# Kernel optimization log

Measured on AMD Instinct MI355X. Metric: run time of the kernel, lower is better.

The kernel has to match this reference:

```python
import jax, jax.numpy as jnp
import numpy as np
from jax import lax

NUM_KP = 17
MAX_PEOPLE = 30
HEAT_THRESH = 0.1
STRIDE = 4  # heatmap -> image coordinate scale

def setup_inputs() -> dict:
    key = jax.random.key(0)
    heatmaps = jax.random.uniform(key, (32, NUM_KP, 256, 256), dtype=jnp.float32)
    return {"heatmaps": heatmaps}

def reference(heatmaps):
    # heatmaps: [B, C, H, W]
    B, C, H, W = heatmaps.shape
    neg_inf = jnp.float32(-jnp.inf)
    # 3x3 max-pool NMS (stride 1, pad 1) batched over all B*C channels at once.
    hmax = lax.reduce_window(
        heatmaps, neg_inf, lax.max,
        window_dimensions=(1, 1, 3, 3),
        window_strides=(1, 1, 1, 1),
        padding=((0, 0), (0, 0), (1, 1), (1, 1)),
    )
    nms = heatmaps * (hmax == heatmaps).astype(heatmaps.dtype)
    # Threshold + descending sort + take top max_people, done as a batched top_k.
    flat = nms.reshape(B, C, H * W)
    masked = jnp.where(flat > HEAT_THRESH, flat, neg_inf)
    scores, idx = lax.top_k(masked, MAX_PEOPLE)          # [B, C, max_people]
    y = idx // W
    x = idx % W
    coords = jnp.stack([x, y], axis=-1).astype(jnp.int32) * STRIDE  # [B,C,max_people,2] as (x,y)*4
    valid = scores > HEAT_THRESH                          # padding mask (original output is ragged)
    return coords, scores, valid
```

## Files before the change

kernel.cpp:

```cpp
#include <hip/hip_runtime.h>
#include <stdint.h>

#define NUM_KP 17
#define BATCH  32
#define HDIM   256
#define WDIM   256
#define NCH    (BATCH * NUM_KP)
#define MAXP   30
#define CAP    8192

#define NBINS  4096
#define QB     125953

__device__ __forceinline__ unsigned long long shfl_down_u64(unsigned long long v, int off) {
    unsigned lo = (unsigned)v, hi = (unsigned)(v >> 32);
    lo = __shfl_down(lo, off);
    hi = __shfl_down(hi, off);
    return ((unsigned long long)hi << 32) | lo;
}
__device__ __forceinline__ unsigned long long shfl_u64(unsigned long long v, int lane) {
    unsigned lo = (unsigned)v, hi = (unsigned)(v >> 32);
    lo = __shfl(lo, lane);
    hi = __shfl(hi, lane);
    return ((unsigned long long)hi << 32) | lo;
}
__device__ __forceinline__ unsigned quant12(float v) {
    int b = (int)(__float_as_uint(v) >> 13) - QB;
    b = b < 1 ? 1 : (b > NBINS - 1 ? NBINS - 1 : b);
    return (unsigned)b;
}

__global__ __launch_bounds__(256)
void pose_fused_kernel(const float* __restrict__ heat, float* __restrict__ out, int out_size) {
    __shared__ unsigned s_buf[CAP];
    __shared__ int s_hist[NBINS];
    __shared__ int s_gsum[256];
    __shared__ unsigned long long s_ref[256];
    __shared__ int s_cnt, s_nref, s_tau;

    const int tid  = threadIdx.x;
    const int chan = blockIdx.x;
    const int wave = tid >> 6;
    const int lane = tid & 63;
    const float NEGINF = -__builtin_inff();
    const float* __restrict__ cp = heat + (size_t)chan * (HDIM * WDIM);

    for (int i = tid; i < NBINS; i += 256) s_hist[i] = 0;
    if (tid == 0) { s_cnt = 0; s_nref = 0; }
    __syncthreads();

    const int r0 = wave << 6;
    const float* colp = cp + (lane << 2);
    const float4 NEG4 = make_float4(NEGINF, NEGINF, NEGINF, NEGINF);

    float4 rm = (r0 > 0) ? *(const float4*)(colp + ((r0 - 1) << 8)) : NEG4;
    float4 rc = *(const float4*)(colp + (r0 << 8));

    for (int rr = 0; rr < 64; ++rr) {
        const int r = r0 + rr;
        float4 rp = (r + 1 < HDIM) ? *(const float4*)(colp + ((r + 1) << 8)) : NEG4;

        float vm0 = fmaxf(rm.x, fmaxf(rc.x, rp.x));
        float vm1 = fmaxf(rm.y, fmaxf(rc.y, rp.y));
        float vm2 = fmaxf(rm.z, fmaxf(rc.z, rp.z));
        float vm3 = fmaxf(rm.w, fmaxf(rc.w, rp.w));
        float left  = __shfl_up(vm3, 1);   if (lane == 0)  left  = NEGINF;
        float right = __shfl_down(vm0, 1); if (lane == 63) right = NEGINF;
        float h0 = fmaxf(left, fmaxf(vm0, vm1));
        float h1 = fmaxf(vm0, fmaxf(vm1, vm2));
        float h2 = fmaxf(vm1, fmaxf(vm2, vm3));
        float h3 = fmaxf(vm2, fmaxf(vm3, right));

        const int base = (r << 8) | (lane << 2);
        if (rc.x > 0.1f && rc.x == h0) {
            int pos = atomicAdd(&s_cnt, 1);
            if (pos < CAP) s_buf[pos] = (quant12(rc.x) << 16) | (unsigned)(base + 0);
        }
        if (rc.y > 0.1f && rc.y == h1) {
            int pos = atomicAdd(&s_cnt, 1);
            if (pos < CAP) s_buf[pos] = (quant12(rc.y) << 16) | (unsigned)(base + 1);
        }
        if (rc.z > 0.1f && rc.z == h2) {
            int pos = atomicAdd(&s_cnt, 1);
            if (pos < CAP) s_buf[pos] = (quant12(rc.z) << 16) | (unsigned)(base + 2);
        }
        if (rc.w > 0.1f && rc.w == h3) {
            int pos = atomicAdd(&s_cnt, 1);
            if (pos < CAP) s_buf[pos] = (quant12(rc.w) << 16) | (unsigned)(base + 3);
        }
        rm = rc; rc = rp;
    }
    __syncthreads();

    const int n = s_cnt < CAP ? s_cnt : CAP;
    for (int i = tid; i < n; i += 256) {
        atomicAdd(&s_hist[s_buf[i] >> 16], 1);
    }
    __syncthreads();

    {
        int s = 0;
        #pragma unroll
        for (int j = 0; j < 16; ++j) s += s_hist[tid * 16 + j];
        s_gsum[tid] = s;
    }
    __syncthreads();
    if (tid == 0) {
        int cum = 0, tau = 0;
        for (int g = 255; g >= 0; --g) {
            int gs = s_gsum[g];
            if (cum + gs >= MAXP) {
                for (int b = g * 16 + 15; b >= g * 16; --b) {
                    cum += s_hist[b];
                    if (cum >= MAXP) { tau = b; break; }
                }
                break;
            }
            cum += gs;
        }
        s_tau = tau;
    }
    __syncthreads();

    const unsigned tau = (unsigned)s_tau;
    for (int i = tid; i < n; i += 256) {
        unsigned p = s_buf[i];
        if ((p >> 16) >= tau) {
            int pos = atomicAdd(&s_nref, 1);
            if (pos < 256) {
                unsigned idx = p & 0xFFFFu;
                float sc = cp[idx];
                s_ref[pos] = ((unsigned long long)__float_as_uint(sc) << 32) | (unsigned)(~idx);
            }
        }
    }
    __syncthreads();
    const int nref = s_nref < 256 ? s_nref : 256;

    if (tid < 64) {
        unsigned long long k0 = (tid       < nref) ? s_ref[tid]       : 0ull;
        unsigned long long k1 = (tid + 64  < nref) ? s_ref[tid + 64]  : 0ull;
        unsigned long long k2 = (tid + 128 < nref) ? s_ref[tid + 128] : 0ull;
        unsigned long long k3 = (tid + 192 < nref) ? s_ref[tid + 192] : 0ull;
        for (int r = 0; r < MAXP; ++r) {
            unsigned long long best = k0; int bs = 0;
            if (k1 > best) { best = k1; bs = 1; }
            if (k2 > best) { best = k2; bs = 2; }
            if (k3 > best) { best = k3; bs = 3; }
            unsigned long long key = best;
            int slot = (bs << 6) | tid;
            #pragma unroll
            for (int off = 32; off > 0; off >>= 1) {
                unsigned long long ok = shfl_down_u64(key, off);
                int os = __shfl_down(slot, off);
                if (ok > key) { key = ok; slot = os; }
            }
            key  = shfl_u64(key, 0);
            slot = __shfl(slot, 0);
            if ((slot & 63) == tid) {
                int which = slot >> 6;
                if      (which == 0) k0 = 0ull;
                else if (which == 1) k1 = 0ull;
                else if (which == 2) k2 = 0ull;
                else                 k3 = 0ull;
            }
            if (tid == 0) {
                float sc, vld; unsigned idx;
                if (key != 0ull) {
                    sc  = __uint_as_float((unsigned)(key >> 32));
                    idx = (~(unsigned)key) & 0xFFFFu;
                    vld = 1.0f;
                } else { sc = NEGINF; idx = 0u; vld = 0.0f; }
                int x = (int)(idx & 255), y = (int)(idx >> 8);
                long long cb = ((long long)chan * MAXP + r) * 2;
                if (cb + 1 < out_size) {
                    out[cb]     = (float)(x * 4);
                    out[cb + 1] = (float)(y * 4);
                }
                long long so = (long long)NCH * MAXP * 2 + (long long)chan * MAXP + r;
                if (so < out_size) out[so] = sc;
                long long vo = (long long)NCH * MAXP * 3 + (long long)chan * MAXP + r;
                if (vo < out_size) out[vo] = vld;
            }
        }
    }
}

extern "C" void kernel_launch(void* const* d_in, const int* in_sizes, int n_in,
                              void* d_out, int out_size, void* d_ws, size_t ws_size,
                              hipStream_t stream) {
    const float* heat = (const float*)d_in[0];
    float* out = (float*)d_out;
    hipLaunchKernelGGL(pose_fused_kernel, dim3(NCH), dim3(256), 0, stream, heat, out, out_size);
}
```

Measured before the change: 259.9 us.

## Use 512 threads, wave-aggregated ballot compaction, and batched row loads in NMS scan

Doubles the block to 512 threads so each wave scans 32 rows instead of 64. Per-element shared atomics are replaced by ballot/popcount compaction with a single atomic per wave per row. Rows are loaded four at a time ahead of use to give more memory-level parallelism. The intent is to cut LDS atomic contention and hide global load latency. In exchange the unrolled loop raises register pressure, and the larger block may limit occupancy given the large shared memory footprint.

After: 238.1 us. -8.4%, faster.

```diff
diff --git a/kernel.cpp b/kernel.cpp
--- a/kernel.cpp
+++ b/kernel.cpp
@@ -12,6 +12,8 @@
 #define NBINS  4096
 #define QB     125953
 
+#define THREADS 512
+
 __device__ __forceinline__ unsigned long long shfl_down_u64(unsigned long long v, int off) {
     unsigned lo = (unsigned)v, hi = (unsigned)(v >> 32);
     lo = __shfl_down(lo, off);
@@ -30,7 +32,7 @@
     return (unsigned)b;
 }
 
-__global__ __launch_bounds__(256)
+__global__ __launch_bounds__(THREADS, 4)
 void pose_fused_kernel(const float* __restrict__ heat, float* __restrict__ out, int out_size) {
     __shared__ unsigned s_buf[CAP];
     __shared__ int s_hist[NBINS];
@@ -45,25 +47,24 @@
     const float NEGINF = -__builtin_inff();
     const float* __restrict__ cp = heat + (size_t)chan * (HDIM * WDIM);
 
-    for (int i = tid; i < NBINS; i += 256) s_hist[i] = 0;
+    for (int i = tid; i < NBINS; i += THREADS) s_hist[i] = 0;
     if (tid == 0) { s_cnt = 0; s_nref = 0; }
     __syncthreads();
 
-    const int r0 = wave << 6;
+    const int r0 = wave << 5;
     const float* colp = cp + (lane << 2);
     const float4 NEG4 = make_float4(NEGINF, NEGINF, NEGINF, NEGINF);
-
-    float4 rm = (r0 > 0) ? *(const float4*)(colp + ((r0 - 1) << 8)) : NEG4;
-    float4 rc = *(const float4*)(colp + (r0 << 8));
-
-    for (int rr = 0; rr < 64; ++rr) {
-        const int r = r0 + rr;
-        float4 rp = (r + 1 < HDIM) ? *(const float4*)(colp + ((r + 1) << 8)) : NEG4;
-
-        float vm0 = fmaxf(rm.x, fmaxf(rc.x, rp.x));
-        float vm1 = fmaxf(rm.y, fmaxf(rc.y, rp.y));
-        float vm2 = fmaxf(rm.z, fmaxf(rc.z, rp.z));
-        float vm3 = fmaxf(rm.w, fmaxf(rc.w, rp.w));
+    const unsigned long long ltmask = (1ull << lane) - 1ull;
+
+    auto LD = [&](int r) -> float4 {
+        return (r >= 0 && r < HDIM) ? *(const float4*)(colp + (r << 8)) : NEG4;
+    };
+
+    auto process = [&](const float4& up, const float4& md, const float4& dn, int r) {
+        float vm0 = fmaxf(up.x, fmaxf(md.x, dn.x));
+        float vm1 = fmaxf(up.y, fmaxf(md.y, dn.y));
+        float vm2 = fmaxf(up.z, fmaxf(md.z, dn.z));
+        float vm3 = fmaxf(up.w, fmaxf(md.w, dn.w));
         float left  = __shfl_up(vm3, 1);   if (lane == 0)  left  = NEGINF;
         float right = __shfl_down(vm0, 1); if (lane == 63) right = NEGINF;
         float h0 = fmaxf(left, fmaxf(vm0, vm1));
@@ -71,34 +72,56 @@
         float h2 = fmaxf(vm1, fmaxf(vm2, vm3));
         float h3 = fmaxf(vm2, fmaxf(vm3, right));
 
+        bool p0 = md.x > 0.1f && md.x == h0;
+        bool p1 = md.y > 0.1f && md.y == h1;
+        bool p2 = md.z > 0.1f && md.z == h2;
+        bool p3 = md.w > 0.1f && md.w == h3;
+        unsigned long long b0 = __ballot(p0), b1 = __ballot(p1);
+        unsigned long long b2 = __ballot(p2), b3 = __ballot(p3);
+        int c0 = __popcll(b0), c1 = __popcll(b1), c2 = __popcll(b2), c3 = __popcll(b3);
+        int tot = c0 + c1 + c2 + c3;
+        int wb = 0;
+        if (lane == 0 && tot > 0) wb = atomicAdd(&s_cnt, tot);
+        wb = __shfl(wb, 0);
+
         const int base = (r << 8) | (lane << 2);
-        if (rc.x > 0.1f && rc.x == h0) {
-            int pos = atomicAdd(&s_cnt, 1);
-            if (pos < CAP) s_buf[pos] = (quant12(rc.x) << 16) | (unsigned)(base + 0);
-        }
-        if (rc.y > 0.1f && rc.y == h1) {
-            int pos = atomicAdd(&s_cnt, 1);
-            if (pos < CAP) s_buf[pos] = (quant12(rc.y) << 16) | (unsigned)(base + 1);
-        }
-        if (rc.z > 0.1f && rc.z == h2) {
-            int pos = atomicAdd(&s_cnt, 1);
-            if (pos < CAP) s_buf[pos] = (quant12(rc.z) << 16) | (unsigned)(base + 2);
-        }
-        if (rc.w > 0.1f && rc.w == h3) {
-            int pos = atomicAdd(&s_cnt, 1);
-            if (pos < CAP) s_buf[pos] = (quant12(rc.w) << 16) | (unsigned)(base + 3);
-        }
-        rm = rc; rc = rp;
+        if (p0) { int pos = wb + __popcll(b0 & ltmask);
+                  if (pos < CAP) s_buf[pos] = (quant12(md.x) << 16) | (unsigned)(base + 0); }
+        if (p1) { int pos = wb + c0 + __popcll(b1 & ltmask);
+                  if (pos < CAP) s_buf[pos] = (quant12(md.y) << 16) | (unsigned)(base + 1); }
+        if (p2) { int pos = wb + c0 + c1 + __popcll(b2 & ltmask);
+                  if (pos < CAP) s_buf[pos] = (quant12(md.z) << 16) | (unsigned)(base + 2); }
+        if (p3) { int pos = wb + c0 + c1 + c2 + __popcll(b3 & ltmask);
+                  if (pos < CAP) s_buf[pos] = (quant12(md.w) << 16) | (unsigned)(base + 3); }
+    };
+
+    float4 rm   = LD(r0 - 1);
+    float4 cur0 = LD(r0 + 0), cur1 = LD(r0 + 1), cur2 = LD(r0 + 2), cur3 = LD(r0 + 3);
+
+    #pragma unroll
+    for (int g = 0; g < 8; ++g) {
+        const int rb = r0 + (g << 2);
+        float4 n0, n1, n2, n3;
+        if (g < 7) {
+            n0 = LD(rb + 4); n1 = LD(rb + 5); n2 = LD(rb + 6); n3 = LD(rb + 7);
+        } else {
+            n0 = LD(rb + 4); n1 = NEG4; n2 = NEG4; n3 = NEG4;
+        }
+        process(rm,   cur0, cur1, rb + 0);
+        process(cur0, cur1, cur2, rb + 1);
+        process(cur1, cur2, cur3, rb + 2);
+        process(cur2, cur3, n0,   rb + 3);
+        rm = cur3; cur0 = n0; cur1 = n1; cur2 = n2; cur3 = n3;
     }
     __syncthreads();
 
     const int n = s_cnt < CAP ? s_cnt : CAP;
-    for (int i = tid; i < n; i += 256) {
+    for (int i = tid; i < n; i += THREADS) {
         atomicAdd(&s_hist[s_buf[i] >> 16], 1);
     }
     __syncthreads();
 
-    {
+    if (tid < 256) {
         int s = 0;
         #pragma unroll
         for (int j = 0; j < 16; ++j) s += s_hist[tid * 16 + j];
@@ -123,7 +146,7 @@
     __syncthreads();
 
     const unsigned tau = (unsigned)s_tau;
-    for (int i = tid; i < n; i += 256) {
+    for (int i = tid; i < n; i += THREADS) {
         unsigned p = s_buf[i];
         if ((p >> 16) >= tau) {
             int pos = atomicAdd(&s_nref, 1);
@@ -191,5 +214,5 @@
                               hipStream_t stream) {
     const float* heat = (const float*)d_in[0];
     float* out = (float*)d_out;
-    hipLaunchKernelGGL(pose_fused_kernel, dim3(NCH), dim3(256), 0, stream, heat, out, out_size);
-}
+    hipLaunchKernelGGL(pose_fused_kernel, dim3(NCH), dim3(THREADS), 0, stream, heat, out, out_size);
+}
```
